# Optimization experiments

Hardware: AMD Instinct MI355X
Metric: run time of the kernel (lower is better)

Reference implementation:

```python
import jax, jax.numpy as jnp
import numpy as np

EPS = 1.0
SIGMA = 1.0
N = 4096

def setup_inputs() -> dict:
    key = jax.random.key(0)
    k1, k2 = jax.random.split(key)
    q = jax.random.uniform(k1, (N, 3), dtype=jnp.float32) * 5.0
    p = jax.random.normal(k2, (N, 3), dtype=jnp.float32) * 0.1
    m = jnp.ones((N, 1), dtype=jnp.float32)
    return {"q": q, "p": p, "m": m, "t": 0}

def reference(q, p, m, t):
    # all-pairs displacement: disp[i, j] = q[i] - q[j], shape [N, N, 3]
    disp = q[:, None, :] - q[None, :, :]
    r = jnp.linalg.norm(disp, axis=2)  # [N, N]
    n = q.shape[0]
    eye = jnp.eye(n, dtype=bool)
    r = jnp.where(eye, 1.0, r)  # fill_diagonal_(1) to avoid div-by-zero

    prefix = 48.0 * EPS
    sigma12 = SIGMA ** 12
    sigma6 = SIGMA ** 6
    inner = sigma12 / r ** 13 - 0.5 * sigma6 / r ** 7
    inner = jnp.where(eye, 0.0, inner)  # fill_diagonal_(0)
    direction = disp / r[:, :, None]
    force = -prefix * inner[:, :, None] * direction  # [N, N, 3]

    dq = p / m
    dp = force.sum(axis=1)  # [N, 3]
    return (dq, dp)
```

## Files before the change

kernel.cpp:

```cpp
#include <hip/hip_runtime.h>

#define N 4096
#define BLOCK 512
#define NB (N / 8)
#define NSTEP (N / 64)

__global__ __launch_bounds__(BLOCK, 4)
void lj_single_kernel(const float* __restrict__ q, const float* __restrict__ p,
                      const float* __restrict__ m, float* __restrict__ out) {
    __shared__ float qs[N * 3];
    const int tid  = threadIdx.x;
    const int lane = tid & 63;
    const int wave = tid >> 6;
    const int i    = blockIdx.x * 8 + wave;

    const float qx = q[i * 3 + 0];
    const float qy = q[i * 3 + 1];
    const float qz = q[i * 3 + 2];

    const int dq_n = (N * 3) / NB;
    float pv = 0.f, mv = 1.f;
    int u = 0;
    if (tid < dq_n) {
        u  = blockIdx.x * dq_n + tid;
        pv = p[u];
        mv = m[u / 3];
    }

    {
        const float4* __restrict__ q4 = (const float4*)q;
        float4* __restrict__ qs4 = (float4*)qs;
        #pragma unroll
        for (int k = 0; k < (N * 3) / 4 / BLOCK; ++k)
            qs4[k * BLOCK + tid] = q4[k * BLOCK + tid];
    }
    __syncthreads();

    float fx = 0.f, fy = 0.f, fz = 0.f;
    const int sdiag = i >> 6;
    const float* __restrict__ qsl = qs + lane * 3;

    #pragma unroll
    for (int st = 0; st < NSTEP; ++st) {
        const float dx = qx - qsl[st * 192 + 0];
        const float dy = qy - qsl[st * 192 + 1];
        const float dz = qz - qsl[st * 192 + 2];
        const float r2 = fmaf(dx, dx, fmaf(dy, dy, dz * dz));
        const float u1 = __builtin_amdgcn_rcpf(r2);
        const float u2 = u1 * u1;
        const float u3 = u2 * u1;
        const float u4 = u2 * u2;
        float s = u4 * fmaf(-48.0f, u3, 24.0f);
        if (st == sdiag)
            s = (st * 64 + lane == i) ? 0.0f : s;
        fx = fmaf(s, dx, fx);
        fy = fmaf(s, dy, fy);
        fz = fmaf(s, dz, fz);
    }

    #pragma unroll
    for (int off = 32; off > 0; off >>= 1) {
        fx += __shfl_xor(fx, off, 64);
        fy += __shfl_xor(fy, off, 64);
        fz += __shfl_xor(fz, off, 64);
    }
    if (lane == 0) {
        out[N * 3 + i * 3 + 0] = fx;
        out[N * 3 + i * 3 + 1] = fy;
        out[N * 3 + i * 3 + 2] = fz;
    }

    if (tid < dq_n)
        out[u] = pv / mv;
}

extern "C" void kernel_launch(void* const* d_in, const int* in_sizes, int n_in,
                              void* d_out, int out_size, void* d_ws, size_t ws_size,
                              hipStream_t stream) {
    const float* q = (const float*)d_in[0];
    const float* p = (const float*)d_in[1];
    const float* m = (const float*)d_in[2];
    float* out = (float*)d_out;

    lj_single_kernel<<<NB, BLOCK, 0, stream>>>(q, p, m, out);
}
```

Before: 15.20 us.

## Compute two particle rows per wave and stage positions as padded float4

Each wave now accumulates forces for two target particles, so every position read from shared memory serves two pair interactions. The block shrinks to 256 threads while still covering 8 rows. Shared positions are repacked from xyz triples into padded float4 entries so each lane reads one vector per step, and the loop unroll drops to 4. The trade-off is 64KB of shared memory instead of 48KB and half as many threads to stage it, which may lengthen the load phase and lower occupancy.

```diff
diff --git a/kernel.cpp b/kernel.cpp
--- a/kernel.cpp
+++ b/kernel.cpp
@@ -1,22 +1,22 @@
 #include <hip/hip_runtime.h>
 
 #define N 4096
-#define BLOCK 512
+#define BLOCK 256
 #define NB (N / 8)
 #define NSTEP (N / 64)
 
-__global__ __launch_bounds__(BLOCK, 4)
+__global__ __launch_bounds__(BLOCK, 2)
 void lj_single_kernel(const float* __restrict__ q, const float* __restrict__ p,
                       const float* __restrict__ m, float* __restrict__ out) {
-    __shared__ float qs[N * 3];
+    __shared__ float4 qs4[N];
     const int tid  = threadIdx.x;
     const int lane = tid & 63;
     const int wave = tid >> 6;
-    const int i    = blockIdx.x * 8 + wave;
+    const int i1   = blockIdx.x * 8 + wave * 2;
+    const int i2   = i1 + 1;
 
-    const float qx = q[i * 3 + 0];
-    const float qy = q[i * 3 + 1];
-    const float qz = q[i * 3 + 2];
+    const float qx1 = q[i1*3+0], qy1 = q[i1*3+1], qz1 = q[i1*3+2];
+    const float qx2 = q[i2*3+0], qy2 = q[i2*3+1], qz2 = q[i2*3+2];
 
     const int dq_n = (N * 3) / NB;
     float pv = 0.f, mv = 1.f;
@@ -29,45 +29,73 @@
 
     {
         const float4* __restrict__ q4 = (const float4*)q;
-        float4* __restrict__ qs4 = (float4*)qs;
         #pragma unroll
-        for (int k = 0; k < (N * 3) / 4 / BLOCK; ++k)
-            qs4[k * BLOCK + tid] = q4[k * BLOCK + tid];
+        for (int k = 0; k < 4; ++k) {
+            const int g  = k * BLOCK + tid;
+            const float4 a = q4[g*3 + 0];
+            const float4 b = q4[g*3 + 1];
+            const float4 c = q4[g*3 + 2];
+            qs4[g*4 + 0] = make_float4(a.x, a.y, a.z, 0.f);
+            qs4[g*4 + 1] = make_float4(a.w, b.x, b.y, 0.f);
+            qs4[g*4 + 2] = make_float4(b.z, b.w, c.x, 0.f);
+            qs4[g*4 + 3] = make_float4(c.y, c.z, c.w, 0.f);
+        }
     }
     __syncthreads();
 
-    float fx = 0.f, fy = 0.f, fz = 0.f;
-    const int sdiag = i >> 6;
-    const float* __restrict__ qsl = qs + lane * 3;
+    float fx1 = 0.f, fy1 = 0.f, fz1 = 0.f;
+    float fx2 = 0.f, fy2 = 0.f, fz2 = 0.f;
+    const int sd1 = i1 >> 6;
+    const int sd2 = i2 >> 6;
+    const float4* __restrict__ qsl = qs4 + lane;
 
-    #pragma unroll
+    #pragma unroll 4
     for (int st = 0; st < NSTEP; ++st) {
-        const float dx = qx - qsl[st * 192 + 0];
-        const float dy = qy - qsl[st * 192 + 1];
-        const float dz = qz - qsl[st * 192 + 2];
-        const float r2 = fmaf(dx, dx, fmaf(dy, dy, dz * dz));
-        const float u1 = __builtin_amdgcn_rcpf(r2);
-        const float u2 = u1 * u1;
-        const float u3 = u2 * u1;
-        const float u4 = u2 * u2;
-        float s = u4 * fmaf(-48.0f, u3, 24.0f);
-        if (st == sdiag)
-            s = (st * 64 + lane == i) ? 0.0f : s;
-        fx = fmaf(s, dx, fx);
-        fy = fmaf(s, dy, fy);
-        fz = fmaf(s, dz, fz);
+        const float4 r = qsl[st * 64];
+        const float dx1 = qx1 - r.x;
+        const float dy1 = qy1 - r.y;
+        const float dz1 = qz1 - r.z;
+        const float r21 = fmaf(dx1, dx1, fmaf(dy1, dy1, dz1 * dz1));
+        const float a1  = __builtin_amdgcn_rcpf(r21);
+        const float b1  = a1 * a1;
+        const float c1  = b1 * a1;
+        const float d1  = b1 * b1;
+        float s1 = d1 * fmaf(-48.0f, c1, 24.0f);
+        const float dx2 = qx2 - r.x;
+        const float dy2 = qy2 - r.y;
+        const float dz2 = qz2 - r.z;
+        const float r22 = fmaf(dx2, dx2, fmaf(dy2, dy2, dz2 * dz2));
+        const float a2  = __builtin_amdgcn_rcpf(r22);
+        const float b2  = a2 * a2;
+        const float c2  = b2 * a2;
+        const float d2  = b2 * b2;
+        float s2 = d2 * fmaf(-48.0f, c2, 24.0f);
+        if (st == sd1) s1 = (st * 64 + lane == i1) ? 0.0f : s1;
+        if (st == sd2) s2 = (st * 64 + lane == i2) ? 0.0f : s2;
+        fx1 = fmaf(s1, dx1, fx1);
+        fy1 = fmaf(s1, dy1, fy1);
+        fz1 = fmaf(s1, dz1, fz1);
+        fx2 = fmaf(s2, dx2, fx2);
+        fy2 = fmaf(s2, dy2, fy2);
+        fz2 = fmaf(s2, dz2, fz2);
     }
 
     #pragma unroll
     for (int off = 32; off > 0; off >>= 1) {
-        fx += __shfl_xor(fx, off, 64);
-        fy += __shfl_xor(fy, off, 64);
-        fz += __shfl_xor(fz, off, 64);
+        fx1 += __shfl_xor(fx1, off, 64);
+        fy1 += __shfl_xor(fy1, off, 64);
+        fz1 += __shfl_xor(fz1, off, 64);
+        fx2 += __shfl_xor(fx2, off, 64);
+        fy2 += __shfl_xor(fy2, off, 64);
+        fz2 += __shfl_xor(fz2, off, 64);
     }
     if (lane == 0) {
-        out[N * 3 + i * 3 + 0] = fx;
-        out[N * 3 + i * 3 + 1] = fy;
-        out[N * 3 + i * 3 + 2] = fz;
+        out[N*3 + i1*3 + 0] = fx1;
+        out[N*3 + i1*3 + 1] = fy1;
+        out[N*3 + i1*3 + 2] = fz1;
+        out[N*3 + i2*3 + 0] = fx2;
+        out[N*3 + i2*3 + 1] = fy2;
+        out[N*3 + i2*3 + 2] = fz2;
     }
 
     if (tid < dq_n)
```

After: 15.22 us. Within noise of the previous version (+0.1%).
